# Kernel optimization log

Measured on AMD Instinct MI355X. Metric: run time of the kernel, lower is better.

Reference implementation:

```python
import jax, jax.numpy as jnp
import numpy as np


def _conv(x, w):
    # NCHW 'same' conv, stride 1 (kernel 7 -> pad 3 each side)
    return jax.lax.conv_general_dilated(
        x, w, window_strides=(1, 1), padding='SAME',
        dimension_numbers=('NCHW', 'OIHW', 'NCHW'))


def _run_dir(x, w_ih, w_hh, b, reverse):
    # x: (B, T, C, H, W); returns (B, T, hid, H, W)
    B, T, C, H, W = x.shape
    hid = w_hh.shape[1]
    # Precompute input-to-gate convs for all timesteps at once (fold T into batch)
    xg = _conv(x.reshape(B * T, C, H, W), w_ih) + b[None, :, None, None]
    xg = xg.reshape(B, T, 4 * hid, H, W).transpose(1, 0, 2, 3, 4)  # (T,B,4hid,H,W)
    h0 = jnp.zeros((B, hid, H, W), x.dtype)
    c0 = jnp.zeros_like(h0)

    def step(carry, g_x):
        h, c = carry
        g = g_x + _conv(h, w_hh)
        i, f, gg, o = jnp.split(g, 4, axis=1)  # PyTorch LSTM gate order
        c = jax.nn.sigmoid(f) * c + jax.nn.sigmoid(i) * jnp.tanh(gg)
        h = jax.nn.sigmoid(o) * jnp.tanh(c)
        return (h, c), h

    _, hs = jax.lax.scan(step, (h0, c0), xg, reverse=reverse)
    return hs.transpose(1, 0, 2, 3, 4)  # (B,T,hid,H,W)


def setup_inputs() -> dict:
    key = jax.random.key(0)
    ks = jax.random.split(key, 6)
    B, T, C, H, W = 8, 16, 3, 32, 32
    hid, K = 64, 7
    s_ih = 1.0 / np.sqrt(C * K * K)
    s_hh = 1.0 / np.sqrt(hid * K * K)
    return {
        'x': jax.random.normal(ks[0], (B, T, C, H, W), jnp.float32),
        'w_ih_f': jax.random.normal(ks[1], (4 * hid, C, K, K), jnp.float32) * s_ih,
        'w_hh_f': jax.random.normal(ks[2], (4 * hid, hid, K, K), jnp.float32) * s_hh,
        'b_f': jnp.zeros((4 * hid,), jnp.float32),
        'w_ih_b': jax.random.normal(ks[3], (4 * hid, C, K, K), jnp.float32) * s_ih,
        'w_hh_b': jax.random.normal(ks[4], (4 * hid, hid, K, K), jnp.float32) * s_hh,
        'b_b': jnp.zeros((4 * hid,), jnp.float32),
    }


def reference(x, w_ih_f, w_hh_f, b_f, w_ih_b, w_hh_b, b_b):
    out_f = _run_dir(x, w_ih_f, w_hh_f, b_f, reverse=False)
    out_b = _run_dir(x, w_ih_b, w_hh_b, b_b, reverse=True)
    # bidirectional concat along channel dim -> (B, T, 2*hid, H, W)
    return jnp.concatenate([out_f, out_b], axis=2)
```

## Files before the change

### kernel.cpp

```cpp
#include <hip/hip_runtime.h>
#include <hip/hip_bf16.h>


#define HP0_B  0
#define HP1_B  3112960
#define C_B    6225920
#define WALL_B 10420224
#define BIAS_B 13860864
#define FLAG_B 13862912

using short8 = __attribute__((ext_vector_type(8))) short;
using f32x4  = __attribute__((ext_vector_type(4))) float;

__device__ __forceinline__ float sigm(float x) { return 1.0f / (1.0f + __expf(-x)); }
__device__ __forceinline__ float tanh_f(float x) {
    x = fminf(fmaxf(x, -30.0f), 30.0f);
    float e = __expf(2.0f * x);
    return (e - 1.0f) / (e + 1.0f);
}

__global__ void detect_dtype(const unsigned int* __restrict__ xw, int* __restrict__ flag) {
    int lane = threadIdx.x;
    int cnt = 0;
    for (int i = 0; i < 4; ++i) {
        unsigned int w = xw[lane * 4 + i];
        unsigned int e = (w >> 7) & 0xFFu;
        cnt += (e >= 0xC0u) ? 1 : 0;
    }
#pragma unroll
    for (int off = 32; off > 0; off >>= 1) cnt += __shfl_down(cnt, off, 64);
    if (lane == 0) *flag = (cnt > 16) ? 1 : 0;
}

__global__ void prep_weights(const void* __restrict__ whhf, const void* __restrict__ whhb,
                             const void* __restrict__ wihf, const void* __restrict__ wihb,
                             const void* __restrict__ bf, const void* __restrict__ bb,
                             short* __restrict__ wall, float* __restrict__ bias_r,
                             const int* __restrict__ flag) {
    int n = blockIdx.x * blockDim.x + threadIdx.x;
    const int fp32 = *flag;
    if (n < 1720320) {
        int icl = n & 31;
        int oc = (n >> 5) & 255;
        int ks = (n >> 13) % 105;
        int d = n / 860160;
        const void* hh = d ? whhb : whhf;
        const void* ih = d ? wihb : wihf;
        float v = 0.0f;
        if (ks < 98) {
            int ky = ks / 14, rr = ks % 14, kc = rr / 7, kx = rr % 7;
            int si = ((oc * 64 + kc * 32 + icl) * 7 + ky) * 7 + kx;
            v = fp32 ? ((const float*)hh)[si] : __bfloat162float(((const __hip_bfloat16*)hh)[si]);
        } else {
            int kx = ks - 98, ky = icl >> 2, ic = icl & 3;
            if (ic < 3 && ky < 7) {
                int si = ((oc * 3 + ic) * 7 + ky) * 7 + kx;
                v = fp32 ? ((const float*)ih)[si] : __bfloat162float(((const __hip_bfloat16*)ih)[si]);
            }
        }
        __hip_bfloat16 hv = __float2bfloat16(v);
        wall[n] = *(short*)&hv;
        return;
    }
    n -= 1720320;
    if (n < 512) {
        const void* src = (n >= 256) ? bb : bf;
        int j = n & 255;
        bias_r[n] = fp32 ? ((const float*)src)[j] : __bfloat162float(((const __hip_bfloat16*)src)[j]);
    }
}

__global__ void zero_state(float* __restrict__ ws_f) {
    int n = blockIdx.x * blockDim.x + threadIdx.x;
    if (n < 2605056) ws_f[n] = 0.0f;
}

__global__ __launch_bounds__(256, 1)
void lstm_step(const void* __restrict__ xin,
               const short* __restrict__ wall,
               const float* __restrict__ bias_r,
               const unsigned short* __restrict__ hp_r,
               unsigned short* __restrict__ hp_w,
               float* __restrict__ c,
               void* __restrict__ out,
               const int* __restrict__ flag, int s) {
    const int ygrp = blockIdx.x;
    const int b = blockIdx.y;
    const int dir = blockIdx.z;
    const int t = dir ? (15 - s) : s;
    const int y0 = ygrp * 2;
    const int tid = threadIdx.x;
    const int w = tid >> 6;
    const int l = tid & 63;
    const int q = l >> 4;
    const int li = l & 15;
    const int fp32 = *flag;
    const int db = dir * 8 + b;

    __shared__ short lds[23040 + 3200];

    {
        const uint4* src = (const uint4*)(hp_r + (size_t)(db * 38 + y0) * 40 * 64);
        for (int i = tid; i < 2560; i += 256) {
            int ic8 = i & 7, col = (i >> 3) % 40, row = i / 320;
            uint4 v = src[i];
            *(uint4*)&lds[(row * 40 + col) * 72 + ic8 * 8] = v;
        }
    }
    for (int i = tid; i < 3200; i += 256) {
        int k = i % 40, cc = (i / 40) % 40, r = i / 1600;
        float v = 0.0f;
        if (k < 28) {
            int ky = k >> 2, ic = k & 3;
            int yin = y0 + r + ky - 3, cin = cc - 3;
            if (ic < 3 && yin >= 0 && yin < 32 && cin >= 0 && cin < 32) {
                size_t gi = (size_t)((b * 16 + t) * 3 + ic) * 1024 + yin * 32 + cin;
                v = fp32 ? ((const float*)xin)[gi]
                         : __bfloat162float(((const __hip_bfloat16*)xin)[gi]);
            }
        }
        __hip_bfloat16 hb = __float2bfloat16(v);
        lds[23040 + i] = *(short*)&hb;
    }
    __syncthreads();

    f32x4 acc[4][4];
    {
        const float* bp = bias_r + dir * 256 + w * 16 + q * 4;
#pragma unroll
        for (int g = 0; g < 4; ++g) {
            f32x4 bv = *(const f32x4*)(bp + g * 64);
#pragma unroll
            for (int nt = 0; nt < 4; ++nt) acc[g][nt] = bv;
        }
    }

    const short* wbase = wall + (size_t)dir * 860160 + ((w * 16 + li) * 32 + q * 8);
    int bh[4], bx[4];
#pragma unroll
    for (int nt = 0; nt < 4; ++nt) {
        int rt = nt >> 1, ct = nt & 1;
        bh[nt] = (rt * 40 + ct * 16 + li) * 72 + q * 8;
        bx[nt] = 23040 + (rt * 40 + ct * 16 + li) * 40 + q * 8;
    }

    auto loadA = [&](short8* A, int ks) {
        const short* p = wbase + (size_t)ks * 8192;
#pragma unroll
        for (int g = 0; g < 4; ++g) A[g] = *(const short8*)(p + g * 2048);
    };
    auto loadB = [&](short8* B, int ks) {
        if (ks < 98) {
            int ky = ks / 14, rr = ks % 14;
            int uoff = ky * 2880 + (rr % 7) * 72 + (rr / 7) * 32;
#pragma unroll
            for (int nt = 0; nt < 4; ++nt) B[nt] = *(const short8*)&lds[bh[nt] + uoff];
        } else {
            int uoff = (ks - 98) * 40;
#pragma unroll
            for (int nt = 0; nt < 4; ++nt) B[nt] = *(const short8*)&lds[bx[nt] + uoff];
        }
    };
    auto mfma16 = [&](short8* A, short8* B) {
#pragma unroll
        for (int g = 0; g < 4; ++g)
#pragma unroll
            for (int nt = 0; nt < 4; ++nt)
                acc[g][nt] = __builtin_amdgcn_mfma_f32_16x16x32_bf16(A[g], B[nt], acc[g][nt], 0, 0, 0);
    };

    short8 A0[4], A1[4], B0[4], B1[4];
    loadA(A0, 0); loadB(B0, 0);
#pragma unroll 1
    for (int ks = 0; ks < 104; ks += 2) {
        loadA(A1, ks + 1); loadB(B1, ks + 1);
        mfma16(A0, B0);
        loadA(A0, ks + 2); loadB(B0, ks + 2);
        mfma16(A1, B1);
    }
    mfma16(A0, B0);

    const int hid0 = w * 16 + q * 4;
#pragma unroll
    for (int nt = 0; nt < 4; ++nt) {
        int y = y0 + (nt >> 1);
        int px = (nt & 1) * 16 + li;
        float* cp = c + (size_t)(db * 1024 + y * 32 + px) * 64 + hid0;
        f32x4 cold = *(const f32x4*)cp;
        f32x4 hv;
#pragma unroll
        for (int r = 0; r < 4; ++r) {
            float iv = sigm(acc[0][nt][r]);
            float fv = sigm(acc[1][nt][r]);
            float gv = tanh_f(acc[2][nt][r]);
            float ov = sigm(acc[3][nt][r]);
            float cn = fv * cold[r] + iv * gv;
            cold[r] = cn;
            hv[r] = ov * tanh_f(cn);
        }
        *(f32x4*)cp = cold;

        ushort4 hu;
        {
            __hip_bfloat16 t0 = __float2bfloat16(hv[0]); hu.x = *(unsigned short*)&t0;
            __hip_bfloat16 t1 = __float2bfloat16(hv[1]); hu.y = *(unsigned short*)&t1;
            __hip_bfloat16 t2 = __float2bfloat16(hv[2]); hu.z = *(unsigned short*)&t2;
            __hip_bfloat16 t3 = __float2bfloat16(hv[3]); hu.w = *(unsigned short*)&t3;
        }
        *(ushort4*)(hp_w + (size_t)((db * 38 + y + 3) * 40 + px + 3) * 64 + hid0) = hu;

        size_t ob = (size_t)((b * 16 + t) * 128 + dir * 64 + hid0) * 1024 + y * 32 + px;
        if (fp32) {
            float* op = (float*)out;
#pragma unroll
            for (int r = 0; r < 4; ++r) op[ob + (size_t)r * 1024] = hv[r];
        } else {
            __hip_bfloat16* op = (__hip_bfloat16*)out;
#pragma unroll
            for (int r = 0; r < 4; ++r) op[ob + (size_t)r * 1024] = __float2bfloat16(hv[r]);
        }
    }
}

extern "C" void kernel_launch(void* const* d_in, const int* in_sizes, int n_in,
                              void* d_out, int out_size, void* d_ws, size_t ws_size,
                              hipStream_t stream) {
    char* wsb = (char*)d_ws;
    unsigned short* hp0 = (unsigned short*)(wsb + HP0_B);
    unsigned short* hp1 = (unsigned short*)(wsb + HP1_B);
    float* c = (float*)(wsb + C_B);
    short* wall = (short*)(wsb + WALL_B);
    float* bias_r = (float*)(wsb + BIAS_B);
    int* flag = (int*)(wsb + FLAG_B);

    detect_dtype<<<1, 64, 0, stream>>>((const unsigned int*)d_in[0], flag);
    prep_weights<<<6722, 256, 0, stream>>>(d_in[2], d_in[5], d_in[1], d_in[4],
                                           d_in[3], d_in[6], wall, bias_r, flag);
    zero_state<<<10176, 256, 0, stream>>>((float*)d_ws);

    for (int s = 0; s < 16; ++s) {
        unsigned short* hr = (s & 1) ? hp1 : hp0;
        unsigned short* hw = (s & 1) ? hp0 : hp1;
        lstm_step<<<dim3(16, 8, 2), 256, 0, stream>>>(d_in[0], wall, bias_r,
                                                      hr, hw, c, d_out, flag, s);
    }
}
```

Before: 663.6 us.

## Retile LSTM step blocks by hidden-channel quarter over eight rows

```diff
diff --git a/kernel.cpp b/kernel.cpp
--- a/kernel.cpp
+++ b/kernel.cpp
@@ -8,6 +8,10 @@
 #define WALL_B 10420224
 #define BIAS_B 13860864
 #define FLAG_B 13862912
+
+#define LDS_XB  40320
+#define LDS_LUT 63360
+#define LDS_SHORTS 63570
 
 using short8 = __attribute__((ext_vector_type(8))) short;
 using f32x4  = __attribute__((ext_vector_type(4))) float;
@@ -40,19 +44,22 @@
     int n = blockIdx.x * blockDim.x + threadIdx.x;
     const int fp32 = *flag;
     if (n < 1720320) {
-        int icl = n & 31;
-        int oc = (n >> 5) & 255;
-        int ks = (n >> 13) % 105;
-        int d = n / 860160;
+        int k = n & 31;
+        int mi = (n >> 5) & 15;
+        int g = (n >> 9) & 3;
+        int ks = (n >> 11) % 105;
+        int hbq = (n >> 11) / 105;
+        int hb = hbq & 3, d = hbq >> 2;
+        int oc = g * 64 + hb * 16 + mi;
         const void* hh = d ? whhb : whhf;
         const void* ih = d ? wihb : wihf;
         float v = 0.0f;
         if (ks < 98) {
             int ky = ks / 14, rr = ks % 14, kc = rr / 7, kx = rr % 7;
-            int si = ((oc * 64 + kc * 32 + icl) * 7 + ky) * 7 + kx;
+            int si = ((oc * 64 + kc * 32 + k) * 7 + ky) * 7 + kx;
             v = fp32 ? ((const float*)hh)[si] : __bfloat162float(((const __hip_bfloat16*)hh)[si]);
         } else {
-            int kx = ks - 98, ky = icl >> 2, ic = icl & 3;
+            int kx = ks - 98, ky = k >> 2, ic = k & 3;
             if (ic < 3 && ky < 7) {
                 int si = ((oc * 3 + ic) * 7 + ky) * 7 + kx;
                 v = fp32 ? ((const float*)ih)[si] : __bfloat162float(((const __hip_bfloat16*)ih)[si]);
@@ -84,11 +91,12 @@
                float* __restrict__ c,
                void* __restrict__ out,
                const int* __restrict__ flag, int s) {
-    const int ygrp = blockIdx.x;
+    const int hb = blockIdx.x & 3;
+    const int ygrp = blockIdx.x >> 2;
     const int b = blockIdx.y;
     const int dir = blockIdx.z;
     const int t = dir ? (15 - s) : s;
-    const int y0 = ygrp * 2;
+    const int Y0 = ygrp * 8;
     const int tid = threadIdx.x;
     const int w = tid >> 6;
     const int l = tid & 63;
@@ -97,36 +105,55 @@
     const int fp32 = *flag;
     const int db = dir * 8 + b;
 
-    __shared__ short lds[23040 + 3200];
+    extern __shared__ short lds[];
+    int* lut = (int*)&lds[LDS_LUT];
+
+    if (tid < 105) {
+        int uoff;
+        if (tid < 98) {
+            int ky = tid / 14, rr = tid % 14, kc = rr / 7, kx = rr % 7;
+            uoff = ky * 2880 + kx * 72 + kc * 32;
+        } else {
+            uoff = LDS_XB + (tid - 98) * 72;
+        }
+        lut[tid] = uoff;
+    }
 
     {
-        const uint4* src = (const uint4*)(hp_r + (size_t)(db * 38 + y0) * 40 * 64);
-        for (int i = tid; i < 2560; i += 256) {
+        const uint4* src = (const uint4*)(hp_r + (size_t)(db * 38 + Y0) * 40 * 64);
+        for (int i = tid; i < 4480; i += 256) {
             int ic8 = i & 7, col = (i >> 3) % 40, row = i / 320;
             uint4 v = src[i];
             *(uint4*)&lds[(row * 40 + col) * 72 + ic8 * 8] = v;
         }
     }
-    for (int i = tid; i < 3200; i += 256) {
-        int k = i % 40, cc = (i / 40) % 40, r = i / 1600;
-        float v = 0.0f;
-        if (k < 28) {
-            int ky = k >> 2, ic = k & 3;
-            int yin = y0 + r + ky - 3, cin = cc - 3;
-            if (ic < 3 && yin >= 0 && yin < 32 && cin >= 0 && cin < 32) {
-                size_t gi = (size_t)((b * 16 + t) * 3 + ic) * 1024 + yin * 32 + cin;
-                v = fp32 ? ((const float*)xin)[gi]
-                         : __bfloat162float(((const __hip_bfloat16*)xin)[gi]);
+    for (int i = tid; i < 5120; i += 256) {
+        int u = i & 15, cc = (i >> 4) % 40, r = i / 640;
+        unsigned int pk = 0;
+#pragma unroll
+        for (int h2 = 0; h2 < 2; ++h2) {
+            int k = 2 * u + h2;
+            float v = 0.0f;
+            if (k < 28) {
+                int ky = k >> 2, ic = k & 3;
+                int yin = Y0 + r + ky - 3, cin = cc - 3;
+                if (ic < 3 && yin >= 0 && yin < 32 && cin >= 0 && cin < 32) {
+                    size_t gi = (size_t)((b * 16 + t) * 3 + ic) * 1024 + yin * 32 + cin;
+                    v = fp32 ? ((const float*)xin)[gi]
+                             : __bfloat162float(((const __hip_bfloat16*)xin)[gi]);
+                }
             }
-        }
-        __hip_bfloat16 hb = __float2bfloat16(v);
-        lds[23040 + i] = *(short*)&hb;
+            __hip_bfloat16 hv = __float2bfloat16(v);
+            pk |= ((unsigned int)*(unsigned short*)&hv) << (16 * h2);
+        }
+        *(unsigned int*)&lds[LDS_XB + (r * 40 + cc) * 72 + 2 * u] = pk;
     }
     __syncthreads();
 
+    const int hid0 = hb * 16 + q * 4;
     f32x4 acc[4][4];
     {
-        const float* bp = bias_r + dir * 256 + w * 16 + q * 4;
+        const float* bp = bias_r + dir * 256 + hid0;
 #pragma unroll
         for (int g = 0; g < 4; ++g) {
             f32x4 bv = *(const f32x4*)(bp + g * 64);
@@ -135,31 +162,21 @@
         }
     }
 
-    const short* wbase = wall + (size_t)dir * 860160 + ((w * 16 + li) * 32 + q * 8);
-    int bh[4], bx[4];
-#pragma unroll
-    for (int nt = 0; nt < 4; ++nt) {
-        int rt = nt >> 1, ct = nt & 1;
-        bh[nt] = (rt * 40 + ct * 16 + li) * 72 + q * 8;
-        bx[nt] = 23040 + (rt * 40 + ct * 16 + li) * 40 + q * 8;
-    }
+    const short* wblk = wall + (size_t)(dir * 4 + hb) * 105 * 2048 + li * 32 + q * 8;
+    int bnt[4];
+#pragma unroll
+    for (int nt = 0; nt < 4; ++nt)
+        bnt[nt] = ((2 * w + (nt >> 1)) * 40 + (nt & 1) * 16 + li) * 72 + q * 8;
 
     auto loadA = [&](short8* A, int ks) {
-        const short* p = wbase + (size_t)ks * 8192;
-#pragma unroll
-        for (int g = 0; g < 4; ++g) A[g] = *(const short8*)(p + g * 2048);
+        const short* p = wblk + (size_t)ks * 2048;
+#pragma unroll
+        for (int g = 0; g < 4; ++g) A[g] = *(const short8*)(p + g * 512);
     };
     auto loadB = [&](short8* B, int ks) {
-        if (ks < 98) {
-            int ky = ks / 14, rr = ks % 14;
-            int uoff = ky * 2880 + (rr % 7) * 72 + (rr / 7) * 32;
-#pragma unroll
-            for (int nt = 0; nt < 4; ++nt) B[nt] = *(const short8*)&lds[bh[nt] + uoff];
-        } else {
-            int uoff = (ks - 98) * 40;
-#pragma unroll
-            for (int nt = 0; nt < 4; ++nt) B[nt] = *(const short8*)&lds[bx[nt] + uoff];
-        }
+        int uoff = lut[ks];
+#pragma unroll
+        for (int nt = 0; nt < 4; ++nt) B[nt] = *(const short8*)&lds[bnt[nt] + uoff];
     };
     auto mfma16 = [&](short8* A, short8* B) {
 #pragma unroll
@@ -180,10 +197,9 @@
     }
     mfma16(A0, B0);
 
-    const int hid0 = w * 16 + q * 4;
 #pragma unroll
     for (int nt = 0; nt < 4; ++nt) {
-        int y = y0 + (nt >> 1);
+        int y = Y0 + 2 * w + (nt >> 1);
         int px = (nt & 1) * 16 + li;
         float* cp = c + (size_t)(db * 1024 + y * 32 + px) * 64 + hid0;
         f32x4 cold = *(const f32x4*)cp;
@@ -238,10 +254,11 @@
                                            d_in[3], d_in[6], wall, bias_r, flag);
     zero_state<<<10176, 256, 0, stream>>>((float*)d_ws);
 
+    const size_t shmem = LDS_SHORTS * sizeof(short);
     for (int s = 0; s < 16; ++s) {
         unsigned short* hr = (s & 1) ? hp1 : hp0;
         unsigned short* hw = (s & 1) ? hp0 : hp1;
-        lstm_step<<<dim3(16, 8, 2), 256, 0, stream>>>(d_in[0], wall, bias_r,
-                                                      hr, hw, c, d_out, flag, s);
-    }
-}
+        lstm_step<<<dim3(16, 8, 2), 256, shmem, stream>>>(d_in[0], wall, bias_r,
+                                                          hr, hw, c, d_out, flag, s);
+    }
+}
```

New measurement: 1.030 ms. 1.55x slower.
